# Optimization experiments

Measured on AMD Instinct MI355X. Metric: run time of the kernel, lower is better.

## Reference

```python
import jax, jax.numpy as jnp
import numpy as np

N_NODES = 100000
N_EDGES = 1600000
STATE_DIM = 128
HIDDEN_DIM = 128
ACTION_DIM = 16


def gcn_conv(x, edge_index, W, b, n_nodes):
    """PyG-style GCNConv: add self-loops, symmetric normalization, x@W then aggregate."""
    xw = x @ W  # [N, H]
    loops = jnp.arange(n_nodes, dtype=edge_index.dtype)
    src = jnp.concatenate([edge_index[0], loops])  # [E+N]
    dst = jnp.concatenate([edge_index[1], loops])
    ones = jnp.ones(src.shape[0], dtype=xw.dtype)
    deg = jax.ops.segment_sum(ones, dst, num_segments=n_nodes)  # degree of target nodes
    dinv = jnp.where(deg > 0, jax.lax.rsqrt(deg), 0.0)
    norm = dinv[src] * dinv[dst]  # [E+N]
    msg = xw[src] * norm[:, None]  # gather + scale (irregular access)
    out = jax.ops.segment_sum(msg, dst, num_segments=n_nodes)  # scatter-aggregate
    return out + b


def setup_inputs() -> dict:
    key = jax.random.key(0)
    ks = jax.random.split(key, 12)
    def lin(k, fan_in, shape):
        bound = 1.0 / np.sqrt(fan_in)
        return jax.random.uniform(k, shape, jnp.float32, -bound, bound)
    return {
        "x": jax.random.normal(ks[0], (N_NODES, STATE_DIM), jnp.float32),
        "edge_index": jax.random.randint(ks[1], (2, N_EDGES), 0, N_NODES, jnp.int64),
        "action": jax.random.normal(ks[2], (N_NODES, ACTION_DIM), jnp.float32),
        "gcn1_w": lin(ks[3], STATE_DIM, (STATE_DIM, HIDDEN_DIM)),
        "gcn1_b": lin(ks[4], STATE_DIM, (HIDDEN_DIM,)),
        "gcn2_w": lin(ks[5], HIDDEN_DIM, (HIDDEN_DIM, HIDDEN_DIM)),
        "gcn2_b": lin(ks[6], HIDDEN_DIM, (HIDDEN_DIM,)),
        "fc1_w": lin(ks[7], HIDDEN_DIM + ACTION_DIM, (HIDDEN_DIM + ACTION_DIM, HIDDEN_DIM)),
        "fc1_b": lin(ks[8], HIDDEN_DIM + ACTION_DIM, (HIDDEN_DIM,)),
        "fc2_w": lin(ks[9], HIDDEN_DIM, (HIDDEN_DIM, 1)),
        "fc2_b": lin(ks[10], HIDDEN_DIM, (1,)),
    }


def reference(x, edge_index, action, gcn1_w, gcn1_b, gcn2_w, gcn2_b, fc1_w, fc1_b, fc2_w, fc2_b):
    n = x.shape[0]
    h = jax.nn.relu(gcn_conv(x, edge_index, gcn1_w, gcn1_b, n))
    h = jax.nn.relu(gcn_conv(h, edge_index, gcn2_w, gcn2_b, n))
    h = jnp.concatenate([h, action], axis=-1)  # [N, H+A]
    h = jax.nn.relu(h @ fc1_w + fc1_b)
    q = h @ fc2_w + fc2_b  # [N, 1]
    return q.squeeze(-1)
```

## Files before the change

kernel.cpp:

```cpp
#include <hip/hip_runtime.h>
#include <hip/hip_bf16.h>

typedef unsigned short u16;
typedef unsigned int   u32;
typedef __attribute__((ext_vector_type(8))) short bf16x8;
typedef __attribute__((ext_vector_type(4))) float f32x4;
typedef __attribute__((ext_vector_type(4))) unsigned int u32x4;

constexpr int NN = 100000;
constexpr int NE = 1600000;
constexpr int D  = 128;
constexpr size_t WS_NEED = 58909184;

constexpr int NBUCK = 196;
constexpr int NBLKA = 512;
constexpr int EPB   = 3136;
constexpr int CAPA  = 48;

__device__ __forceinline__ float bf2f(u16 u){ union{u32 i;float f;}v; v.i=((u32)u)<<16; return v.f; }
__device__ __forceinline__ float2 bfp(u32 u){ union{u32 i;float f;}a,b; a.i=u<<16; b.i=u&0xffff0000u; return make_float2(a.f,b.f); }
__device__ __forceinline__ u16 f2bf(float f){ union{float f;u32 i;}v; v.f=f; u32 r=v.i + 0x7fffu + ((v.i>>16)&1u); return (u16)(r>>16); }
__device__ __forceinline__ u32 pk2(float a, float b){ return (u32)f2bf(a) | ((u32)f2bf(b)<<16); }

__global__ void detect_kernel(const u32* __restrict__ xw, const int* __restrict__ ei,
                              int* __restrict__ flagf, int* __restrict__ flage){
  __shared__ int shf[256];
  __shared__ int she[256];
  int t = threadIdx.x;
  int cnt = 0;
  for(int i = 0; i < 16; i++){
    u32 w = xw[(t*16 + i) * 256];
    int e = (int)((w >> 7) & 0xFFu);
    cnt += (e >= 64 && e <= 160) ? 1 : 0;
  }
  int nz = 0;
  for(int i = 0; i < 8; i++){
    int k = t*8 + i;
    long long w = 1 + ((long long)k * (2LL*NE - 2)) / 2048;
    nz += (ei[(int)(w | 1)] != 0) ? 1 : 0;
  }
  shf[t] = cnt; she[t] = nz;
  __syncthreads();
  for(int off=128; off>0; off>>=1){
    if(t<off){ shf[t]+=shf[t+off]; she[t]+=she[t+off]; }
    __syncthreads();
  }
  if(t==0){ flagf[0] = (shf[0] < 3000) ? 1 : 0; flage[0] = (she[0] == 0) ? 1 : 0; }
}

__global__ void prep_kernel(const void* __restrict__ w1, const void* __restrict__ w2,
    const void* __restrict__ fw1, const void* __restrict__ b1, const void* __restrict__ b2,
    const void* __restrict__ fb1, const void* __restrict__ fw2, const void* __restrict__ fb2,
    const int* __restrict__ flagf,
    u16* __restrict__ WT1, u16* __restrict__ WT2, u16* __restrict__ WTF, float* __restrict__ BF)
{
  const int ff = flagf[0];
  int i = blockIdx.x*256 + threadIdx.x;
  auto cv = [&](const void* p, int idx)->float{
    return ff ? ((const float*)p)[idx] : bf2f(((const u16*)p)[idx]);
  };
  if(i < 16384){
    int k = i >> 7, d = i & 127;
    WT1[d*128 + k] = f2bf(cv(w1, i));
  }else if(i < 32768){
    int j = i - 16384; int k = j >> 7, d = j & 127;
    WT2[d*128 + k] = f2bf(cv(w2, j));
  }else if(i < 51200){
    int j = i - 32768; int k = j >> 7, d = j & 127;
    WTF[d*144 + k] = f2bf(cv(fw1, j));
  }else if(i < 51713){
    int j = i - 51200;
    if(j < 128)       BF[j]   = cv(b1, j);
    else if(j < 256)  BF[j]   = cv(b2, j-128);
    else if(j < 384)  BF[j]   = cv(fb1, j-256);
    else if(j < 512)  BF[j]   = cv(fw2, j-384);
    else              BF[512] = cv(fb2, 0);
  }
}

__global__ void fill1_kernel(u16* __restrict__ out, int n){
  int i = blockIdx.x*blockDim.x + threadIdx.x;
  if(i < n) out[i] = 0x3F80;
}

__global__ __launch_bounds__(512) void passA_kernel(
    const int* __restrict__ ei, const int* __restrict__ flage,
    u32* __restrict__ ebuf, u32* __restrict__ counts)
{
  __shared__ u32 hist[NBUCK];
  int t = threadIdx.x;
  if(t < NBUCK) hist[t] = 0;
  __syncthreads();
  const int f = flage[0];
  const int eb = blockIdx.x * EPB;
  const u32 cbase = blockIdx.x * NBUCK;
  for(int g = t; g < EPB/4; g += 512){
    int e4 = eb + g*4;
    if(e4 >= NE) break;
    int sv[4], dv[4];
    if(f){
      uint4 sa = *(const uint4*)(ei + 2*(size_t)e4);
      uint4 sb = *(const uint4*)(ei + 2*(size_t)e4 + 4);
      uint4 da = *(const uint4*)(ei + 2*(size_t)(NE + e4));
      uint4 db = *(const uint4*)(ei + 2*(size_t)(NE + e4) + 4);
      sv[0]=(int)sa.x; sv[1]=(int)sa.z; sv[2]=(int)sb.x; sv[3]=(int)sb.z;
      dv[0]=(int)da.x; dv[1]=(int)da.z; dv[2]=(int)db.x; dv[3]=(int)db.z;
    }else{
      uint4 sa = *(const uint4*)(ei + e4);
      uint4 da = *(const uint4*)(ei + NE + e4);
      sv[0]=(int)sa.x; sv[1]=(int)sa.y; sv[2]=(int)sa.z; sv[3]=(int)sa.w;
      dv[0]=(int)da.x; dv[1]=(int)da.y; dv[2]=(int)da.z; dv[3]=(int)da.w;
    }
    #pragma unroll
    for(int q=0;q<4;q++){
      int s = sv[q], d = dv[q];
      if((u32)s >= (u32)NN || (u32)d >= (u32)NN) continue;
      int b = d >> 9;
      u32 rank = atomicAdd(&hist[b], 1u);
      if(rank < CAPA) ebuf[(size_t)(cbase + b)*CAPA + rank] = (u32)s | ((u32)(d & 511) << 17);
    }
  }
  __syncthreads();
  if(t < NBUCK){
    u32 c = hist[t];
    counts[t*NBLKA + blockIdx.x] = (c < CAPA) ? c : CAPA;
  }
}

__global__ void scan196_kernel(const u32* __restrict__ counts, int* __restrict__ bases){
  __shared__ int sh[NBUCK];
  int t = threadIdx.x;
  if(t < NBUCK){
    const uint4* p = (const uint4*)(counts + (size_t)t*NBLKA);
    int tot = 0;
    for(int c = 0; c < NBLKA/4; c++){ uint4 v = p[c]; tot += (int)(v.x + v.y + v.z + v.w); }
    sh[t] = tot;
  }
  __syncthreads();
  if(t == 0){
    int acc = 0;
    for(int b = 0; b < NBUCK; b++){ int v = sh[b]; sh[b] = acc; acc += v; }
  }
  __syncthreads();
  if(t < NBUCK) bases[t] = sh[t];
}

__global__ __launch_bounds__(512) void passB_kernel(
    const u32* __restrict__ ebuf, const u32* __restrict__ counts, const int* __restrict__ bases,
    int* __restrict__ deg, int* __restrict__ off, float* __restrict__ dinv,
    int* __restrict__ srcs)
{
  __shared__ int cnt[512];
  __shared__ int nodeoff[512];
  __shared__ int pos[512];
  __shared__ int wsum[8], wpre[8];
  const int t = threadIdx.x;
  const int b = blockIdx.x;
  const int v0 = b << 9;

  cnt[t] = 0;
  __syncthreads();

  const int cnum = (int)counts[b*NBLKA + t];
  const u32* cp = ebuf + (size_t)(t*NBUCK + b)*CAPA;

  {
    int i = 0;
    for(; i + 4 <= cnum; i += 4){
      uint4 r = *(const uint4*)(cp + i);
      atomicAdd(&cnt[r.x >> 17], 1); atomicAdd(&cnt[r.y >> 17], 1);
      atomicAdd(&cnt[r.z >> 17], 1); atomicAdd(&cnt[r.w >> 17], 1);
    }
    for(; i < cnum; i++) atomicAdd(&cnt[cp[i] >> 17], 1);
  }
  __syncthreads();

  const int myc = cnt[t];
  const int lane = t & 63, wid = t >> 6;
  int v = myc;
  #pragma unroll
  for(int o = 1; o < 64; o <<= 1){
    int u = __shfl_up(v, o, 64);
    if(lane >= o) v += u;
  }
  if(lane == 63) wsum[wid] = v;
  __syncthreads();
  if(t == 0){
    int acc = 0;
    #pragma unroll
    for(int w = 0; w < 8; w++){ wpre[w] = acc; acc += wsum[w]; }
  }
  __syncthreads();
  const int excl = v - myc + wpre[wid];
  nodeoff[t] = excl;
  pos[t] = 0;
  __syncthreads();

  const int gb = bases[b];

  {
    int i = 0;
    for(; i + 4 <= cnum; i += 4){
      uint4 rq = *(const uint4*)(cp + i);
      u32 rr[4] = {rq.x, rq.y, rq.z, rq.w};
      #pragma unroll
      for(int q = 0; q < 4; q++){
        int ld = rr[q] >> 17;
        int r = atomicAdd(&pos[ld], 1);
        srcs[gb + nodeoff[ld] + r] = (int)(rr[q] & 0x1FFFFu);
      }
    }
    for(; i < cnum; i++){
      u32 rec = cp[i];
      int ld = rec >> 17;
      int r = atomicAdd(&pos[ld], 1);
      srcs[gb + nodeoff[ld] + r] = (int)(rec & 0x1FFFFu);
    }
  }

  int vn = v0 + t;
  if(vn < NN){
    deg[vn] = myc;
    off[vn] = gb + excl;
    dinv[vn] = rsqrtf((float)(myc + 1));
  }
}

__global__ __launch_bounds__(256) void gemm1_kernel(
    const void* __restrict__ A1, const u16* __restrict__ WT,
    const int* __restrict__ flagf, const float* __restrict__ dscale,
    u16* __restrict__ out, int n)
{
  const int tid = threadIdx.x;
  const int nb  = blockIdx.x * 64;
  const int ff  = flagf[0];
  const int wave = tid >> 6;
  const int lane = tid & 63;
  const int quad = lane >> 4;
  const int lm   = lane & 15;

  int arow = nb + wave*16 + lm; if(arow >= n) arow = n-1;

  bf16x8 afr[4];
  if(!ff){
    const u16* xr = (const u16*)A1 + (size_t)arow*128 + quad*8;
    #pragma unroll
    for(int k=0;k<4;k++) afr[k] = *(const bf16x8*)(xr + 32*k);
  }else{
    const float* xr = (const float*)A1 + (size_t)arow*128 + quad*8;
    #pragma unroll
    for(int k=0;k<4;k++){
      float4 p0 = *(const float4*)(xr + 32*k);
      float4 p1 = *(const float4*)(xr + 32*k + 4);
      union{u32x4 u; bf16x8 v;} cvv;
      cvv.u = (u32x4){pk2(p0.x,p0.y), pk2(p0.z,p0.w), pk2(p1.x,p1.y), pk2(p1.z,p1.w)};
      afr[k] = cvv.v;
    }
  }

  f32x4 acc[8];
  #pragma unroll
  for(int t=0;t<8;t++) acc[t] = (f32x4){0.f,0.f,0.f,0.f};

  #pragma unroll
  for(int ki = 0; ki < 4; ki++){
    int kk = ki*32 + quad*8;
    #pragma unroll
    for(int t=0;t<8;t++){
      bf16x8 b = *(const bf16x8*)(WT + (size_t)(t*16 + lm)*128 + kk);
      acc[t] = __builtin_amdgcn_mfma_f32_16x16x32_bf16(afr[ki], b, acc[t], 0, 0, 0);
    }
  }

  const int node0 = nb + wave*16 + quad*4;
  #pragma unroll
  for(int r=0;r<4;r++){
    int gr = node0 + r;
    if(gr < n){
      float dv = dscale[gr];
      #pragma unroll
      for(int t=0;t<8;t++){
        out[(size_t)gr*D + t*16 + lm] = f2bf(acc[t][r]*dv);
      }
    }
  }
}

#define ACC8(r)  { float2 f_;                       \
    f_ = bfp((r).x); a0 += f_.x; a1 += f_.y;        \
    f_ = bfp((r).y); a2 += f_.x; a3 += f_.y;        \
    f_ = bfp((r).z); a4 += f_.x; a5 += f_.y;        \
    f_ = bfp((r).w); a6 += f_.x; a7 += f_.y; }

template<bool FINAL>
__global__ __launch_bounds__(256) void fused_kernel(
    const int* __restrict__ off, const int* __restrict__ deg,
    const int* __restrict__ srcs, const float* __restrict__ dinv,
    const u16* __restrict__ xw, const float* __restrict__ biasf,
    const u16* __restrict__ WT, const float* __restrict__ fb1,
    const float* __restrict__ qwf, const float* __restrict__ qbf,
    const void* __restrict__ action, const int* __restrict__ flagf,
    void* __restrict__ out)
{
  constexpr int K  = FINAL ? 144 : 128;
  constexpr int KT = FINAL ? 160 : 128;
  constexpr int KP = KT + 8;
  constexpr int NKI = KT/32;
  __shared__ u16 Hs[16*KP];
  __shared__ float qred[FINAL ? 64 : 4];

  const int tid  = threadIdx.x;
  const int node0 = blockIdx.x * 16;
  const int nl   = tid >> 4;
  const int l16  = tid & 15;
  const int node = node0 + nl;

  const int wave = tid >> 6;
  const int lane = tid & 63;
  const int quad = lane >> 4;
  const int lm   = lane & 15;

  const int j0 = off[node];
  const int j1 = j0 + deg[node];
  float a0=0.f,a1=0.f,a2=0.f,a3=0.f,a4=0.f,a5=0.f,a6=0.f,a7=0.f;
  const u16* __restrict__ xl = xw + 8*l16;

  int j = j0;
  int s0=0, s1=0, s2=0, s3=0;
  const bool pre = (j + 4 <= j1);
  if(pre){
    s0 = __builtin_nontemporal_load(&srcs[j]);
    s1 = __builtin_nontemporal_load(&srcs[j+1]);
    s2 = __builtin_nontemporal_load(&srcs[j+2]);
    s3 = __builtin_nontemporal_load(&srcs[j+3]);
  }
  for(; j + 8 <= j1; j += 4){
    uint4 r0 = *(const uint4*)(xl + (size_t)s0*D);
    uint4 r1 = *(const uint4*)(xl + (size_t)s1*D);
    uint4 r2 = *(const uint4*)(xl + (size_t)s2*D);
    uint4 r3 = *(const uint4*)(xl + (size_t)s3*D);
    s0 = __builtin_nontemporal_load(&srcs[j+4]);
    s1 = __builtin_nontemporal_load(&srcs[j+5]);
    s2 = __builtin_nontemporal_load(&srcs[j+6]);
    s3 = __builtin_nontemporal_load(&srcs[j+7]);
    ACC8(r0); ACC8(r1); ACC8(r2); ACC8(r3);
  }
  if(pre){
    uint4 r0 = *(const uint4*)(xl + (size_t)s0*D);
    uint4 r1 = *(const uint4*)(xl + (size_t)s1*D);
    uint4 r2 = *(const uint4*)(xl + (size_t)s2*D);
    uint4 r3 = *(const uint4*)(xl + (size_t)s3*D);
    ACC8(r0); ACC8(r1); ACC8(r2); ACC8(r3);
    j += 4;
  }
  for(; j < j1; j++){
    int s = __builtin_nontemporal_load(&srcs[j]);
    uint4 r = *(const uint4*)(xl + (size_t)s*D);
    ACC8(r);
  }

  uint4 ps = *(const uint4*)(xl + (size_t)node*D);
  ACC8(ps);
  const float dv = dinv[node];
  float4 bA = *(const float4*)(biasf + 8*l16);
  float4 bB = *(const float4*)(biasf + 8*l16 + 4);
  float o0 = fmaxf(fmaf(dv,a0,bA.x), 0.f);
  float o1 = fmaxf(fmaf(dv,a1,bA.y), 0.f);
  float o2 = fmaxf(fmaf(dv,a2,bA.z), 0.f);
  float o3 = fmaxf(fmaf(dv,a3,bA.w), 0.f);
  float o4 = fmaxf(fmaf(dv,a4,bB.x), 0.f);
  float o5 = fmaxf(fmaf(dv,a5,bB.y), 0.f);
  float o6 = fmaxf(fmaf(dv,a6,bB.z), 0.f);
  float o7 = fmaxf(fmaf(dv,a7,bB.w), 0.f);
  uint4 pkd;
  pkd.x = pk2(o0,o1); pkd.y = pk2(o2,o3); pkd.z = pk2(o4,o5); pkd.w = pk2(o6,o7);

  u16* Hp = Hs + nl*KP;
  *(uint4*)(Hp + 8*l16) = pkd;

  if(FINAL){
    const int ff = flagf[0];
    if(ff){
      if(l16 < 4){
        const float* af = (const float*)action + (size_t)node*16 + l16*4;
        float4 p = *(const float4*)af;
        uint2 q; q.x = pk2(p.x,p.y); q.y = pk2(p.z,p.w);
        *(uint2*)(Hp + 128 + 4*l16) = q;
      }
    }else{
      if(l16 < 2){
        uint4 v = *(const uint4*)((const u16*)action + (size_t)node*16 + 8*l16);
        *(uint4*)(Hp + 128 + 8*l16) = v;
      }
    }
    if(l16 >= 14){
      *(uint4*)(Hp + 144 + 8*(l16-14)) = make_uint4(0,0,0,0);
    }
  }

  bf16x8 bfr[NKI][2];
  #pragma unroll
  for(int ki = 0; ki < NKI; ki++){
    int kk = ki*32 + quad*8;
    #pragma unroll
    for(int tt=0; tt<2; tt++){
      int col = (wave*2 + tt)*16 + lm;
      bfr[ki][tt] = (bf16x8){0,0,0,0,0,0,0,0};
      if(!FINAL || kk < K)
        bfr[ki][tt] = *(const bf16x8*)(WT + (size_t)col*K + kk);
    }
  }
  __syncthreads();

  const u16* Ab = Hs + lm*KP;
  f32x4 acc[2];
  acc[0] = (f32x4){0.f,0.f,0.f,0.f};
  acc[1] = (f32x4){0.f,0.f,0.f,0.f};

  #pragma unroll
  for(int ki = 0; ki < NKI; ki++){
    int kk = ki*32 + quad*8;
    bf16x8 a = *(const bf16x8*)(Ab + kk);
    acc[0] = __builtin_amdgcn_mfma_f32_16x16x32_bf16(a, bfr[ki][0], acc[0], 0, 0, 0);
    acc[1] = __builtin_amdgcn_mfma_f32_16x16x32_bf16(a, bfr[ki][1], acc[1], 0, 0, 0);
  }

  const int rbase = quad*4;
  if(!FINAL){
    #pragma unroll
    for(int r=0;r<4;r++){
      int gn = node0 + rbase + r;
      float dvr = dinv[gn];
      #pragma unroll
      for(int tt=0;tt<2;tt++){
        int col = (wave*2 + tt)*16 + lm;
        ((u16*)out)[(size_t)gn*D + col] = f2bf(acc[tt][r]*dvr);
      }
    }
  }else{
    float qp[4] = {0.f,0.f,0.f,0.f};
    #pragma unroll
    for(int tt=0;tt<2;tt++){
      int col = (wave*2 + tt)*16 + lm;
      float bv = fb1[col];
      float qw = qwf[col];
      #pragma unroll
      for(int r=0;r<4;r++){
        float h = fmaxf(acc[tt][r] + bv, 0.f);
        qp[r] += h * qw;
      }
    }
    #pragma unroll
    for(int r=0;r<4;r++){
      #pragma unroll
      for(int o=1; o<16; o<<=1) qp[r] += __shfl_xor(qp[r], o, 16);
    }
    if(lm == 0){
      #pragma unroll
      for(int r=0;r<4;r++) qred[wave*16 + rbase + r] = qp[r];
    }
    __syncthreads();
    if(tid < 16){
      float q = qred[tid] + qred[16+tid] + qred[32+tid] + qred[48+tid] + qbf[0];
      int gn = node0 + tid;
      const int ff = flagf[0];
      if(ff) ((float*)out)[gn] = q;
      else   ((u16*)out)[gn]  = f2bf(q);
    }
  }
}

extern "C" void kernel_launch(void* const* d_in, const int* in_sizes, int n_in,
                              void* d_out, int out_size, void* d_ws, size_t ws_size,
                              hipStream_t stream)
{
  bool meta_ok = (n_in >= 11) && (in_sizes[0] == NN*D) && (in_sizes[1] == 2*NE)
              && (in_sizes[2] == NN*16) && (out_size == NN);
  if(!meta_ok){
    fill1_kernel<<<(NN+255)/256, 256, 0, stream>>>((u16*)d_out, NN);
    return;
  }
  if(ws_size < WS_NEED) return;

  const void* x      = d_in[0];
  const int*  ei     = (const int*)d_in[1];
  const void* action = d_in[2];
  const void* w1     = d_in[3];
  const void* b1     = d_in[4];
  const void* w2     = d_in[5];
  const void* b2     = d_in[6];
  const void* fw1    = d_in[7];
  const void* fb1    = d_in[8];
  const void* fw2    = d_in[9];
  const void* fb2    = d_in[10];

  char* ws = (char*)d_ws;
  int*   DEG    = (int*)(ws + 0);
  int*   OFF    = (int*)(ws + 400128);
  float* DINV   = (float*)(ws + 800256);
  int*   FLAGE  = (int*)(ws + 1204480);
  int*   FLAGF  = (int*)(ws + 1204544);
  u16*   WT1    = (u16*)(ws + 1204608);
  u16*   WT2    = (u16*)(ws + 1237376);
  u16*   WTF    = (u16*)(ws + 1270144);
  float* BF     = (float*)(ws + 1307008);
  int*   SRCS   = (int*)(ws + 1309184);
  u16*   F0     = (u16*)(ws + 7709184);
  u16*   F1     = (u16*)(ws + 33309184);
  u32*   EBUF   = (u32*)(ws + 33309184);
  u32*   COUNTS = (u32*)(ws + 52576768);
  int*   BASES  = (int*)(ws + 52978176);

  detect_kernel<<<1, 256, 0, stream>>>((const u32*)x, ei, FLAGF, FLAGE);

  passA_kernel<<<NBLKA, 512, 0, stream>>>(ei, FLAGE, EBUF, COUNTS);
  scan196_kernel<<<1, 256, 0, stream>>>(COUNTS, BASES);
  passB_kernel<<<NBUCK, 512, 0, stream>>>(EBUF, COUNTS, BASES, DEG, OFF, DINV, SRCS);

  prep_kernel<<<203, 256, 0, stream>>>(w1, w2, fw1, b1, b2, fb1, fw2, fb2, FLAGF,
                                       WT1, WT2, WTF, BF);

  gemm1_kernel<<<(NN+63)/64, 256, 0, stream>>>(x, WT1, FLAGF, DINV, F0, NN);

  fused_kernel<false><<<(NN+15)/16, 256, 0, stream>>>(
      OFF, DEG, SRCS, DINV, F0, BF, WT2, nullptr, nullptr, nullptr, nullptr, FLAGF, F1);

  fused_kernel<true><<<(NN+15)/16, 256, 0, stream>>>(
      OFF, DEG, SRCS, DINV, F1, BF+128, WTF, BF+256, BF+384, BF+512, action, FLAGF, d_out);
}
```

Baseline: 335.0 us.

## Fold detection and bucket scan into prep, passA and passB to cut launches

Removes the single-block detect and scan196 kernels. Each prep block now recomputes the float-format flag itself, and each passA block checks its own edges to decide the int64 layout locally. Each passB block computes its global base by summing the counts of earlier buckets. This takes two serial small launches off the critical path, at the cost of redundant per-block reads. Deciding the int64 layout per block from a local sample is less robust than the old global check.

```diff
diff --git a/kernel.cpp b/kernel.cpp
--- a/kernel.cpp
+++ b/kernel.cpp
@@ -22,40 +22,38 @@
 __device__ __forceinline__ u16 f2bf(float f){ union{float f;u32 i;}v; v.f=f; u32 r=v.i + 0x7fffu + ((v.i>>16)&1u); return (u16)(r>>16); }
 __device__ __forceinline__ u32 pk2(float a, float b){ return (u32)f2bf(a) | ((u32)f2bf(b)<<16); }
 
-__global__ void detect_kernel(const u32* __restrict__ xw, const int* __restrict__ ei,
-                              int* __restrict__ flagf, int* __restrict__ flage){
-  __shared__ int shf[256];
-  __shared__ int she[256];
-  int t = threadIdx.x;
+__global__ void fill1_kernel(u16* __restrict__ out, int n){
+  int i = blockIdx.x*blockDim.x + threadIdx.x;
+  if(i < n) out[i] = 0x3F80;
+}
+
+__global__ __launch_bounds__(512) void prep_kernel(
+    const u32* __restrict__ xw,
+    const void* __restrict__ w1, const void* __restrict__ w2,
+    const void* __restrict__ fw1, const void* __restrict__ b1, const void* __restrict__ b2,
+    const void* __restrict__ fb1, const void* __restrict__ fw2, const void* __restrict__ fb2,
+    int* __restrict__ flagf,
+    u16* __restrict__ WT1, u16* __restrict__ WT2, u16* __restrict__ WTF, float* __restrict__ BF)
+{
+  __shared__ int sh[512];
+  const int t = threadIdx.x;
   int cnt = 0;
-  for(int i = 0; i < 16; i++){
-    u32 w = xw[(t*16 + i) * 256];
+  #pragma unroll
+  for(int i = 0; i < 8; i++){
+    u32 w = xw[(t*8 + i) * 256];
     int e = (int)((w >> 7) & 0xFFu);
     cnt += (e >= 64 && e <= 160) ? 1 : 0;
   }
-  int nz = 0;
-  for(int i = 0; i < 8; i++){
-    int k = t*8 + i;
-    long long w = 1 + ((long long)k * (2LL*NE - 2)) / 2048;
-    nz += (ei[(int)(w | 1)] != 0) ? 1 : 0;
-  }
-  shf[t] = cnt; she[t] = nz;
-  __syncthreads();
-  for(int off=128; off>0; off>>=1){
-    if(t<off){ shf[t]+=shf[t+off]; she[t]+=she[t+off]; }
+  sh[t] = cnt;
+  __syncthreads();
+  for(int o = 256; o > 0; o >>= 1){
+    if(t < o) sh[t] += sh[t + o];
     __syncthreads();
   }
-  if(t==0){ flagf[0] = (shf[0] < 3000) ? 1 : 0; flage[0] = (she[0] == 0) ? 1 : 0; }
-}
-
-__global__ void prep_kernel(const void* __restrict__ w1, const void* __restrict__ w2,
-    const void* __restrict__ fw1, const void* __restrict__ b1, const void* __restrict__ b2,
-    const void* __restrict__ fb1, const void* __restrict__ fw2, const void* __restrict__ fb2,
-    const int* __restrict__ flagf,
-    u16* __restrict__ WT1, u16* __restrict__ WT2, u16* __restrict__ WTF, float* __restrict__ BF)
-{
-  const int ff = flagf[0];
-  int i = blockIdx.x*256 + threadIdx.x;
+  const int ff = (sh[0] < 3000) ? 1 : 0;
+  if(blockIdx.x == 0 && t == 0) flagf[0] = ff;
+
+  int i = blockIdx.x*512 + t;
   auto cv = [&](const void* p, int idx)->float{
     return ff ? ((const float*)p)[idx] : bf2f(((const u16*)p)[idx]);
   };
@@ -78,21 +76,25 @@
   }
 }
 
-__global__ void fill1_kernel(u16* __restrict__ out, int n){
-  int i = blockIdx.x*blockDim.x + threadIdx.x;
-  if(i < n) out[i] = 0x3F80;
-}
-
 __global__ __launch_bounds__(512) void passA_kernel(
-    const int* __restrict__ ei, const int* __restrict__ flage,
+    const int* __restrict__ ei,
     u32* __restrict__ ebuf, u32* __restrict__ counts)
 {
   __shared__ u32 hist[NBUCK];
-  int t = threadIdx.x;
+  __shared__ int fsh;
+  const int t = threadIdx.x;
+  const int eb = blockIdx.x * EPB;
   if(t < NBUCK) hist[t] = 0;
-  __syncthreads();
-  const int f = flage[0];
-  const int eb = blockIdx.x * EPB;
+  if(t == 0) fsh = 0;
+  __syncthreads();
+  {
+    int k = eb + t; if(k >= NE) k = t;
+    int nz = (ei[2*(size_t)k + 1] != 0) ? 1 : 0;
+    if(__any(nz)){ if((t & 63) == 0) atomicOr(&fsh, 1); }
+  }
+  __syncthreads();
+  const int f = (fsh == 0) ? 1 : 0;
+
   const u32 cbase = blockIdx.x * NBUCK;
   for(int g = t; g < EPB/4; g += 512){
     int e4 = eb + g*4;
@@ -127,26 +129,8 @@
   }
 }
 
-__global__ void scan196_kernel(const u32* __restrict__ counts, int* __restrict__ bases){
-  __shared__ int sh[NBUCK];
-  int t = threadIdx.x;
-  if(t < NBUCK){
-    const uint4* p = (const uint4*)(counts + (size_t)t*NBLKA);
-    int tot = 0;
-    for(int c = 0; c < NBLKA/4; c++){ uint4 v = p[c]; tot += (int)(v.x + v.y + v.z + v.w); }
-    sh[t] = tot;
-  }
-  __syncthreads();
-  if(t == 0){
-    int acc = 0;
-    for(int b = 0; b < NBUCK; b++){ int v = sh[b]; sh[b] = acc; acc += v; }
-  }
-  __syncthreads();
-  if(t < NBUCK) bases[t] = sh[t];
-}
-
 __global__ __launch_bounds__(512) void passB_kernel(
-    const u32* __restrict__ ebuf, const u32* __restrict__ counts, const int* __restrict__ bases,
+    const u32* __restrict__ ebuf, const u32* __restrict__ counts,
     int* __restrict__ deg, int* __restrict__ off, float* __restrict__ dinv,
     int* __restrict__ srcs)
 {
@@ -154,12 +138,27 @@
   __shared__ int nodeoff[512];
   __shared__ int pos[512];
   __shared__ int wsum[8], wpre[8];
+  __shared__ int gbs;
   const int t = threadIdx.x;
   const int b = blockIdx.x;
   const int v0 = b << 9;
+  const int lane = t & 63, wid = t >> 6;
 
   cnt[t] = 0;
-  __syncthreads();
+
+  int part = 0;
+  for(int q = 0; q < b; q++) part += (int)counts[q*NBLKA + t];
+  int rp = part;
+  #pragma unroll
+  for(int o = 1; o < 64; o <<= 1) rp += __shfl_xor(rp, o, 64);
+  if(lane == 0) wsum[wid] = rp;
+  __syncthreads();
+  if(t == 0){
+    int a = 0;
+    #pragma unroll
+    for(int w = 0; w < 8; w++) a += wsum[w];
+    gbs = a;
+  }
 
   const int cnum = (int)counts[b*NBLKA + t];
   const u32* cp = ebuf + (size_t)(t*NBUCK + b)*CAPA;
@@ -176,7 +175,6 @@
   __syncthreads();
 
   const int myc = cnt[t];
-  const int lane = t & 63, wid = t >> 6;
   int v = myc;
   #pragma unroll
   for(int o = 1; o < 64; o <<= 1){
@@ -196,7 +194,7 @@
   pos[t] = 0;
   __syncthreads();
 
-  const int gb = bases[b];
+  const int gb = gbs;
 
   {
     int i = 0;
@@ -498,7 +496,6 @@
   int*   DEG    = (int*)(ws + 0);
   int*   OFF    = (int*)(ws + 400128);
   float* DINV   = (float*)(ws + 800256);
-  int*   FLAGE  = (int*)(ws + 1204480);
   int*   FLAGF  = (int*)(ws + 1204544);
   u16*   WT1    = (u16*)(ws + 1204608);
   u16*   WT2    = (u16*)(ws + 1237376);
@@ -509,16 +506,13 @@
   u16*   F1     = (u16*)(ws + 33309184);
   u32*   EBUF   = (u32*)(ws + 33309184);
   u32*   COUNTS = (u32*)(ws + 52576768);
-  int*   BASES  = (int*)(ws + 52978176);
-
-  detect_kernel<<<1, 256, 0, stream>>>((const u32*)x, ei, FLAGF, FLAGE);
-
-  passA_kernel<<<NBLKA, 512, 0, stream>>>(ei, FLAGE, EBUF, COUNTS);
-  scan196_kernel<<<1, 256, 0, stream>>>(COUNTS, BASES);
-  passB_kernel<<<NBUCK, 512, 0, stream>>>(EBUF, COUNTS, BASES, DEG, OFF, DINV, SRCS);
-
-  prep_kernel<<<203, 256, 0, stream>>>(w1, w2, fw1, b1, b2, fb1, fw2, fb2, FLAGF,
-                                       WT1, WT2, WTF, BF);
+
+  prep_kernel<<<102, 512, 0, stream>>>((const u32*)x, w1, w2, fw1, b1, b2, fb1, fw2, fb2,
+                                       FLAGF, WT1, WT2, WTF, BF);
+
+  passA_kernel<<<NBLKA, 512, 0, stream>>>(ei, EBUF, COUNTS);
+
+  passB_kernel<<<NBUCK, 512, 0, stream>>>(EBUF, COUNTS, DEG, OFF, DINV, SRCS);
 
   gemm1_kernel<<<(NN+63)/64, 256, 0, stream>>>(x, WT1, FLAGF, DINV, F0, NN);
 
```

After: 337.5 us. Within noise of the previous version (+0.7%).
